# Kernel optimization log

Measured on AMD Instinct MI355X. Metric: run time of the kernel, lower is better.

Reference implementation:

```python
import jax, jax.numpy as jnp
import numpy as np

D = 200; H = 4; DH = D // H
N_ETYPE = 38; N_NTYPE = 4
B = 256; L = 1024; E = B * L
NODES_PER_G = 200; N = B * NODES_PER_G


def _bn(x, g, b):
    # BatchNorm1d in training mode: batch stats over rows (biased variance, eps=1e-5)
    m = x.mean(axis=0)
    v = x.var(axis=0)
    return (x - m) * jax.lax.rsqrt(v + 1e-5) * g + b


def setup_inputs():
    key = jax.random.key(0)
    ks = jax.random.split(key, 24)
    f = lambda k, s: jax.random.normal(k, s, jnp.float32) * 0.02
    head = jax.random.randint(ks[0], (E,), 0, N)
    tail = (head + 1 + jax.random.randint(ks[1], (E,), 0, N - 1)) % N  # guaranteed no self-loops
    return {
        "x": jax.random.normal(ks[2], (N, D), jnp.float32),
        "node_feature_extra": jax.random.normal(ks[3], (N, D), jnp.float32),
        "sent_vec_r": jax.random.normal(ks[4], (B, D), jnp.float32),
        "We1": f(ks[5], (N_ETYPE + 1 + 2 * N_NTYPE, D)), "be1": jnp.zeros((D,), jnp.float32),
        "ge1": jnp.ones((D,), jnp.float32), "bte1": jnp.zeros((D,), jnp.float32),
        "We2": f(ks[6], (D, D)), "be2": jnp.zeros((D,), jnp.float32),
        "Wa1": f(ks[7], (2 * D, D)), "ba1": jnp.zeros((D,), jnp.float32),
        "ga1": jnp.ones((D,), jnp.float32), "bta1": jnp.zeros((D,), jnp.float32),
        "Wa2": f(ks[8], (D, D)), "ba2": jnp.zeros((D,), jnp.float32),
        "Watt": f(ks[9], (D, D)),
        "Wk": f(ks[10], (2 * D, D)), "bk": jnp.zeros((D,), jnp.float32),
        "Wm": f(ks[11], (2 * D, D)), "bm": jnp.zeros((D,), jnp.float32),
        "Wq": f(ks[12], (D, D)), "bq": jnp.zeros((D,), jnp.float32),
        "Wo1": f(ks[13], (D, D)), "bo1": jnp.zeros((D,), jnp.float32),
        "go1": jnp.ones((D,), jnp.float32), "bto1": jnp.zeros((D,), jnp.float32),
        "Wo2": f(ks[14], (D, D)), "bo2": jnp.zeros((D,), jnp.float32),
        "edge_index": jnp.stack([head, tail]),
        "edge_type": jax.random.randint(ks[15], (E,), 0, N_ETYPE),
        "node_type": jax.random.randint(ks[16], (N,), 0, N_NTYPE),
        "edges_per_graph": L,
    }


def reference(x, node_feature_extra, sent_vec_r, We1, be1, ge1, bte1, We2, be2,
              Wa1, ba1, ga1, bta1, Wa2, ba2, Watt, Wk, bk, Wm, bm, Wq, bq,
              Wo1, bo1, go1, bto1, Wo2, bo2,
              edge_index, edge_type, node_type, edges_per_graph):
    E_, N_ = edge_index.shape[1], x.shape[0]
    src, dst = edge_index[0], edge_index[1]
    x_head, x_tail = x[src], x[dst]
    x_fact = x_tail - x_head
    nt = N_ETYPE + 1
    # original does this segment-mean on detached CPU numpy -> no gradient path
    xf = jax.lax.stop_gradient(x_fact)
    sums = jax.ops.segment_sum(xf, edge_type, num_segments=nt)
    cnts = jax.ops.segment_sum(jnp.ones((E_,), x.dtype), edge_type, num_segments=nt)
    result = (sums / jnp.maximum(cnts, 1.0)[:, None])[edge_type]  # [E, D]
    # one-hot edge/node-type features for real edges + self edges
    edge_vec = jax.nn.one_hot(edge_type, nt, dtype=x.dtype)
    self_edge_vec = jnp.zeros((N_, nt), x.dtype).at[:, N_ETYPE].set(1.0)
    ht = jnp.concatenate([jax.nn.one_hot(node_type[src], N_NTYPE, dtype=x.dtype),
                          jax.nn.one_hot(node_type[dst], N_NTYPE, dtype=x.dtype)], 1)
    sh = jax.nn.one_hot(node_type, N_NTYPE, dtype=x.dtype)
    feat = jnp.concatenate([jnp.concatenate([edge_vec, ht], 1),
                            jnp.concatenate([self_edge_vec, sh, sh], 1)], 0)  # [E+N, 47]
    emb = jax.nn.relu(_bn(feat @ We1 + be1, ge1, bte1)) @ We2 + be2  # edge_encoder, [E+N, D]
    emb_e, emb_self = emb[:E_], emb[E_:]
    # edge_encoder_again on cat([emb_e, result]); split matmul avoids the [E,2D] concat
    h2 = _bn(emb_e @ Wa1[:D] + result @ Wa1[D:] + ba1, ga1, bta1)
    R = jax.nn.relu(h2) @ Wa2 + ba2  # [E, D]
    # per-graph attention: Q rows within a graph are identical (repeated sent_vec),
    # so the LxL softmax has identical rows -> compute one row per graph and broadcast.
    Bg = E_ // edges_per_graph
    Rg = R.reshape(Bg, edges_per_graph, D)
    q = sent_vec_r @ Watt  # [B, D]
    scores = jnp.einsum('bd,bld->bl', q, Rg) / jnp.sqrt(jnp.asarray(D, x.dtype))
    attn = jax.nn.softmax(scores, axis=1)
    upd = jnp.einsum('bl,bld->bd', attn, Rg)
    updated_R = jnp.broadcast_to(upd[:, None, :], Rg.shape).reshape(E_, D)
    edge_attr = jnp.concatenate([updated_R, emb_self], 0)
    # append self-loops (input edge_index has none, matching remove_self_loops)
    loop = jnp.arange(N_, dtype=src.dtype)
    src_all = jnp.concatenate([src, loop])
    dst_all = jnp.concatenate([dst, loop])
    x_i, x_j = x[dst_all], x[src_all]
    key_ = (x_i @ Wk[:D] + edge_attr @ Wk[D:] + bk).reshape(-1, H, DH)
    msg = (x_j @ Wm[:D] + edge_attr @ Wm[D:] + bm).reshape(-1, H, DH)
    qry = ((x_j @ Wq + bq) / jnp.sqrt(jnp.asarray(DH, x.dtype))).reshape(-1, H, DH)
    sc = (qry * key_).sum(-1)  # [E+N, H]
    # segment softmax grouped by source node (every segment non-empty due to self-loops)
    smax = jax.ops.segment_max(sc, src_all, num_segments=N_)
    ex = jnp.exp(sc - smax[src_all])
    den = jax.ops.segment_sum(ex, src_all, num_segments=N_)
    alpha = ex / den[src_all]
    cnt = jax.ops.segment_sum(jnp.ones((src_all.shape[0],), x.dtype), src_all, num_segments=N_)
    alpha = alpha * cnt[src_all][:, None]
    m = (msg * alpha[:, :, None]).reshape(-1, D)
    aggr = jax.ops.segment_sum(m, dst_all, num_segments=N_)  # scatter-add at targets
    return jax.nn.relu(_bn(aggr @ Wo1 + bo1, go1, bto1)) @ Wo2 + bo2
```

## Files before the change

### kernel.cpp

```cpp
#include <hip/hip_runtime.h>

#define D     200
#define H     4
#define DH    50
#define NE    38
#define NTY   4
#define NC    608
#define NCT   612
#define BG    256
#define LG    1024
#define EE    262144
#define NN    51200
#define EA    313344
#define NB    200

#define NTILES 13
#define KSTEPS 7
#define NMATS  8
#define SLICE_SHORTS 13312
#define NCHUNK 26

typedef __attribute__((ext_vector_type(4))) float  f32x4;
typedef __attribute__((ext_vector_type(8))) short  bf16x8;

__device__ __forceinline__ short bf_hi(float f) {
    unsigned u = __float_as_uint(f);
    unsigned r = u + 0x7fffu + ((u >> 16) & 1u);
    return (short)(r >> 16);
}
__device__ __forceinline__ float bf_f(short s) {
    return __uint_as_float(((unsigned)(unsigned short)s) << 16);
}

__global__ __launch_bounds__(256) void k_hist(const int* __restrict__ ei, const int* __restrict__ et,
                                              const int* __restrict__ nt, int* hist, int* outdeg, int* indeg,
                                              int* hcnt) {
    int e = blockIdx.x * 256 + threadIdx.x;
    if (e >= EE) return;
    int s = ei[e], d = ei[EE + e];
    int c = et[e] * 16 + nt[s] * 4 + nt[d];
    atomicAdd(&hist[c], 1);
    atomicAdd(&outdeg[s], 1);
    atomicAdd(&indeg[d], 1);
    atomicAdd(&hcnt[(e >> 10) * NC + c], 1);
}

__global__ __launch_bounds__(256) void k_ntcnt(const int* __restrict__ nt, int* ntcnt) {
    __shared__ int loc[NTY];
    int t = threadIdx.x;
    if (t < NTY) loc[t] = 0;
    __syncthreads();
    int n = blockIdx.x * 256 + t;
    if (n < NN) atomicAdd(&loc[nt[n]], 1);
    __syncthreads();
    if (t < NTY) atomicAdd(&ntcnt[t], loc[t]);
}

__global__ void k_tcnt(const int* __restrict__ hist, int* tcnt) {
    int t = threadIdx.x;
    if (t < NE) { int s = 0; for (int i = 0; i < 16; i++) s += hist[t*16 + i]; tcnt[t] = s; }
}

__global__ __launch_bounds__(256) void k_coef(const int* __restrict__ ei, const int* __restrict__ et,
                                              float* coef) {
    int e = blockIdx.x * 256 + threadIdx.x;
    if (e >= EE) return;
    int s = ei[e], d = ei[EE + e], t = et[e];
    unsafeAtomicAdd(&coef[(size_t)d * NE + t],  1.f);
    unsafeAtomicAdd(&coef[(size_t)s * NE + t], -1.f);
}

__global__ __launch_bounds__(256) void k_xfsum3(const float* __restrict__ x, const float* __restrict__ coef,
                                                float* sums) {
    const int CH = NN / 256;
    int t = threadIdx.x;
    int n0 = blockIdx.x * CH;
    float acc[NE];
    #pragma unroll
    for (int m = 0; m < NE; m++) acc[m] = 0.f;
    if (t < D) {
        for (int k = 0; k < CH; k++) {
            int n = n0 + k;
            float xv = x[(size_t)n * D + t];
            const float* cf = coef + (size_t)n * NE;
            #pragma unroll
            for (int m = 0; m < NE; m++) acc[m] += cf[m] * xv;
        }
        #pragma unroll
        for (int m = 0; m < NE; m++)
            if (acc[m] != 0.f) unsafeAtomicAdd(&sums[m * D + t], acc[m]);
    }
}

__global__ __launch_bounds__(256) void k_scan_a(const int* __restrict__ a, const int* __restrict__ b,
                                                int* bsA, int* bsB) {
    __shared__ int redA[4], redB[4];
    int t = threadIdx.x, blk = blockIdx.x;
    int i = blk * 256 + t;
    int va = a[i], vb = b[i];
    for (int o = 1; o < 64; o <<= 1) { va += __shfl_xor(va, o); vb += __shfl_xor(vb, o); }
    int wave = t >> 6, lane = t & 63;
    if (lane == 0) { redA[wave] = va; redB[wave] = vb; }
    __syncthreads();
    if (t == 0) {
        bsA[blk] = redA[0] + redA[1] + redA[2] + redA[3];
        bsB[blk] = redB[0] + redB[1] + redB[2] + redB[3];
    }
}

__global__ __launch_bounds__(256) void k_scan_b(int* bsA, int* bsB, int* aoff, int* boff) {
    __shared__ int pa[256], pb[256];
    int t = threadIdx.x;
    int va = (t < NB) ? bsA[t] : 0;
    int vb = (t < NB) ? bsB[t] : 0;
    pa[t] = va; pb[t] = vb;
    __syncthreads();
    for (int off = 1; off < 256; off <<= 1) {
        int xa = (t >= off) ? pa[t - off] : 0;
        int xb = (t >= off) ? pb[t - off] : 0;
        __syncthreads();
        pa[t] += xa; pb[t] += xb;
        __syncthreads();
    }
    if (t < NB) { bsA[t] = pa[t] - va; bsB[t] = pb[t] - vb; }
    if (t == NB - 1) { aoff[NN] = pa[t]; boff[NN] = pb[t]; }
}

__global__ __launch_bounds__(256) void k_scan_c(const int* __restrict__ a, const int* __restrict__ b,
                                                const int* __restrict__ bsA, const int* __restrict__ bsB,
                                                int* aoff, int* boff, int* acur, int* bcur) {
    __shared__ int wsA[4], wsB[4];
    int t = threadIdx.x, blk = blockIdx.x;
    int i = blk * 256 + t;
    int va = a[i], vb = b[i];
    int wave = t >> 6, lane = t & 63;
    int sa = va, sb = vb;
    for (int o = 1; o < 64; o <<= 1) {
        int xa = __shfl_up(sa, o);
        int xb = __shfl_up(sb, o);
        if (lane >= o) { sa += xa; sb += xb; }
    }
    if (lane == 63) { wsA[wave] = sa; wsB[wave] = sb; }
    __syncthreads();
    int baseA = bsA[blk], baseB = bsB[blk];
    #pragma unroll
    for (int wv = 0; wv < 3; wv++) {
        if (wv < wave) { baseA += wsA[wv]; baseB += wsB[wv]; }
    }
    int ea = baseA + sa - va;
    int eb = baseB + sb - vb;
    aoff[i] = ea; acur[i] = ea;
    boff[i] = eb; bcur[i] = eb;
}

__global__ __launch_bounds__(256) void k_scatter(const int* __restrict__ ei, int* scur, int* dcur,
                                                 int* slist, int* dlist) {
    int e = blockIdx.x * 256 + threadIdx.x;
    if (e >= EE) return;
    int s = ei[e], d = ei[EE + e];
    slist[atomicAdd(&scur[s], 1)] = e;
    dlist[atomicAdd(&dcur[d], 1)] = e;
}

__global__ __launch_bounds__(256) void k_combos1(const float* __restrict__ We1, const float* __restrict__ be1,
                                                 const int* __restrict__ hist, const int* __restrict__ ntcnt,
                                                 float* __restrict__ h1, float* bn1) {
    int c = blockIdx.x, d = threadIdx.x;
    if (d >= D) return;
    float v, w;
    if (c < NC) {
        int etp = c >> 4, ts = (c >> 2) & 3, td = c & 3;
        v = We1[etp*D + d] + We1[(39+ts)*D + d] + We1[(43+td)*D + d] + be1[d];
        w = (float)hist[c];
    } else {
        int t = c - NC;
        v = We1[38*D + d] + We1[(39+t)*D + d] + We1[(43+t)*D + d] + be1[d];
        w = (float)ntcnt[t];
    }
    h1[c*D + d] = v;
    unsafeAtomicAdd(&bn1[d], w * v);
    unsafeAtomicAdd(&bn1[D + d], w * v * v);
}

__global__ __launch_bounds__(256) void k_combos2(const float* __restrict__ h1, const float* __restrict__ bn1,
                                                 const float* __restrict__ ge1, const float* __restrict__ bte1,
                                                 const float* __restrict__ We2, const float* __restrict__ be2,
                                                 float* __restrict__ embE, float* __restrict__ embS) {
    __shared__ float v[D];
    int c = blockIdx.x, t = threadIdx.x;
    if (t < D) {
        float cnt = (float)(EE + NN);
        float m = bn1[t] / cnt;
        float var = bn1[D + t] / cnt - m * m;
        float r = rsqrtf(var + 1e-5f);
        float u = (h1[c*D + t] - m) * r * ge1[t] + bte1[t];
        v[t] = fmaxf(u, 0.f);
    }
    __syncthreads();
    if (t < D) {
        float acc = be2[t];
        for (int k = 0; k < D; k++) acc += v[k] * We2[k*D + t];
        if (c < NC) embE[c*D + t] = acc; else embS[(c-NC)*D + t] = acc;
    }
}

__global__ __launch_bounds__(256) void k_combos3(const float* __restrict__ embE, const float* __restrict__ sumsxf,
                                                 const int* __restrict__ tcnt, const float* __restrict__ Wa1,
                                                 const float* __restrict__ ba1, const int* __restrict__ hist,
                                                 float* __restrict__ h2, float* bn2) {
    __shared__ float a[2*D];
    int c = blockIdx.x, t = threadIdx.x;
    int etp = c >> 4;
    if (t < D) {
        a[t] = embE[c*D + t];
        float cn = fmaxf((float)tcnt[etp], 1.f);
        a[D + t] = sumsxf[etp*D + t] / cn;
    }
    __syncthreads();
    if (t < D) {
        float acc = ba1[t];
        for (int k = 0; k < 2*D; k++) acc += a[k] * Wa1[k*D + t];
        h2[c*D + t] = acc;
        float w = (float)hist[c];
        unsafeAtomicAdd(&bn2[t], w * acc);
        unsafeAtomicAdd(&bn2[D + t], w * acc * acc);
    }
}

__global__ __launch_bounds__(256) void k_combos4(const float* __restrict__ h2, const float* __restrict__ bn2,
                                                 const float* __restrict__ ga1, const float* __restrict__ bta1,
                                                 const float* __restrict__ Wa2, const float* __restrict__ ba2,
                                                 float* __restrict__ Rc, float* __restrict__ RcT) {
    __shared__ float v[D];
    int c = blockIdx.x, t = threadIdx.x;
    if (t < D) {
        float inv = 1.f / (float)EE;
        float m = bn2[t] * inv;
        float var = bn2[D + t] * inv - m * m;
        float r = rsqrtf(var + 1e-5f);
        float u = (h2[c*D + t] - m) * r * ga1[t] + bta1[t];
        v[t] = fmaxf(u, 0.f);
    }
    __syncthreads();
    if (t < D) {
        float acc = ba2[t];
        for (int k = 0; k < D; k++) acc += v[k] * Wa2[k*D + t];
        Rc[c*D + t] = acc;
        RcT[(size_t)t * NC + c] = acc;
    }
}

__global__ __launch_bounds__(512) void k_attn(const float* __restrict__ qs,
                                              const float* __restrict__ Rc, const float* __restrict__ RcT,
                                              const int* __restrict__ hcnt, float* __restrict__ upd) {
    __shared__ float q[D];
    __shared__ float w[NC];
    __shared__ float red[16];
    __shared__ float part[8][D];
    int b = blockIdx.x, t = threadIdx.x;
    int wave = t >> 6, lane = t & 63;
    if (t < D) q[t] = qs[b*D + t];
    __syncthreads();
    {
        float s0a = 0.f, s0b = 0.f, s0c = 0.f, s0d = 0.f;
        float s1a = 0.f, s1b = 0.f, s1c = 0.f, s1d = 0.f;
        for (int k = 0; k < D; k += 4) {
            float q0 = q[k], q1 = q[k+1], q2 = q[k+2], q3 = q[k+3];
            const float* r = RcT + (size_t)k * NC;
            s0a += q0 * r[t];
            s0b += q1 * r[NC + t];
            s0c += q2 * r[2*NC + t];
            s0d += q3 * r[3*NC + t];
            if (t < NC - 512) {
                s1a += q0 * r[t + 512];
                s1b += q1 * r[NC + t + 512];
                s1c += q2 * r[2*NC + t + 512];
                s1d += q3 * r[3*NC + t + 512];
            }
        }
        w[t] = (s0a + s0b) + (s0c + s0d);
        if (t < NC - 512) w[t + 512] = (s1a + s1b) + (s1c + s1d);
    }
    __syncthreads();
    float mx = -1e30f;
    for (int c = t; c < NC; c += 512) mx = fmaxf(mx, w[c]);
    for (int o = 32; o; o >>= 1) mx = fmaxf(mx, __shfl_xor(mx, o));
    if (lane == 0) red[wave] = mx;
    __syncthreads();
    mx = red[0];
    #pragma unroll
    for (int i = 1; i < 8; i++) mx = fmaxf(mx, red[i]);
    float sm = 0.f;
    for (int c = t; c < NC; c += 512) {
        float wv = (float)hcnt[b * NC + c] * __expf(w[c] - mx);
        w[c] = wv;
        sm += wv;
    }
    for (int o = 32; o; o >>= 1) sm += __shfl_xor(sm, o);
    if (lane == 0) red[8 + wave] = sm;
    __syncthreads();
    float tot = red[8];
    #pragma unroll
    for (int i = 1; i < 8; i++) tot += red[8 + i];
    float inv = 1.f / tot;
    float a4[4] = {0.f, 0.f, 0.f, 0.f};
    for (int c = wave * (NC/8); c < (wave + 1) * (NC/8); c++) {
        float wv = w[c];
        const float* r = Rc + c * D;
        #pragma unroll
        for (int j = 0; j < 4; j++) { int dd = lane + 64*j; if (dd < D) a4[j] += wv * r[dd]; }
    }
    #pragma unroll
    for (int j = 0; j < 4; j++) { int dd = lane + 64*j; if (dd < D) part[wave][dd] = a4[j]; }
    __syncthreads();
    if (t < D) {
        float s = part[0][t];
        #pragma unroll
        for (int i = 1; i < 8; i++) s += part[i][t];
        upd[b*D + t] = s * inv;
    }
}

__global__ __launch_bounds__(256) void k_packW(const float* __restrict__ Wk, const float* __restrict__ Wm,
                                               const float* __restrict__ Wq, const float* __restrict__ Wo1,
                                               const float* __restrict__ Wo2, const float* __restrict__ Watt,
                                               short* __restrict__ Bpk) {
    int blk = blockIdx.x;
    int mat = blk / (NTILES * KSTEPS);
    int rem = blk - mat * (NTILES * KSTEPS);
    int ks = rem / NTILES, nt = rem - ks * NTILES;
    const float* W = (mat == 0) ? Wk : (mat == 1) ? Wm : (mat == 2) ? Wq : (mat == 3) ? Wo1 :
                     (mat == 4) ? Wo2 : (mat == 5) ? Watt : (mat == 6) ? (Wk + D*D) : (Wm + D*D);
    int t = threadIdx.x;
    for (int idx = t; idx < 1024; idx += 256) {
        int split = idx >> 9;
        int lane = (idx & 511) >> 3;
        int j = idx & 7;
        int n = nt * 16 + (lane & 15);
        int k = ks * 32 + ((lane >> 4) << 3) + j;
        float v = (k < D && n < D) ? W[k * D + n] : 0.f;
        short h = bf_hi(v);
        short out = split ? bf_hi(v - bf_f(h)) : h;
        Bpk[(size_t)blk * 1024 + idx] = out;
    }
}

__device__ __forceinline__ void stage_load(const short* __restrict__ g, int w, int lane, f32x4 rg[7]) {
    #pragma unroll
    for (int i = 0; i < 7; i++) {
        int c = w + 4 * i;
        if (c < NCHUNK) rg[i] = *(const f32x4*)((const char*)g + c * 1024 + lane * 16);
    }
}
__device__ __forceinline__ void stage_write(short* l, int w, int lane, const f32x4 rg[7]) {
    #pragma unroll
    for (int i = 0; i < 7; i++) {
        int c = w + 4 * i;
        if (c < NCHUNK) *(f32x4*)((char*)l + c * 1024 + lane * 16) = rg[i];
    }
}

__device__ __forceinline__ void load_afrag(const float* __restrict__ A, int row, int quad, int ks,
                                           int preop, const float* __restrict__ bnacc, float invCnt,
                                           const float* __restrict__ g, const float* __restrict__ bb,
                                           bf16x8& ah, bf16x8& al) {
    int k0 = ks * 32 + quad * 8;
    float v[8];
    if (k0 < D) {
        const float* src = A + (size_t)row * D + k0;
        float4 p0 = *(const float4*)src;
        float4 p1 = *(const float4*)(src + 4);
        v[0]=p0.x; v[1]=p0.y; v[2]=p0.z; v[3]=p0.w;
        v[4]=p1.x; v[5]=p1.y; v[6]=p1.z; v[7]=p1.w;
        if (preop) {
            float4 m0 = *(const float4*)(bnacc + k0);
            float4 m1 = *(const float4*)(bnacc + k0 + 4);
            float4 q0 = *(const float4*)(bnacc + D + k0);
            float4 q1 = *(const float4*)(bnacc + D + k0 + 4);
            float4 g0 = *(const float4*)(g + k0);
            float4 g1 = *(const float4*)(g + k0 + 4);
            float4 b0 = *(const float4*)(bb + k0);
            float4 b1 = *(const float4*)(bb + k0 + 4);
            float mm[8] = {m0.x,m0.y,m0.z,m0.w,m1.x,m1.y,m1.z,m1.w};
            float qq[8] = {q0.x,q0.y,q0.z,q0.w,q1.x,q1.y,q1.z,q1.w};
            float gg[8] = {g0.x,g0.y,g0.z,g0.w,g1.x,g1.y,g1.z,g1.w};
            float bv[8] = {b0.x,b0.y,b0.z,b0.w,b1.x,b1.y,b1.z,b1.w};
            #pragma unroll
            for (int j = 0; j < 8; j++) {
                float mj = mm[j] * invCnt;
                float var = qq[j] * invCnt - mj * mj;
                float rs = rsqrtf(var + 1e-5f);
                float s = rs * gg[j];
                v[j] = fmaxf(v[j] * s + (bv[j] - mj * s), 0.f);
            }
        }
    } else {
        #pragma unroll
        for (int j = 0; j < 8; j++) v[j] = 0.f;
    }
    #pragma unroll
    for (int j = 0; j < 8; j++) {
        short h = bf_hi(v[j]);
        ah[j] = h;
        al[j] = bf_hi(v[j] - bf_f(h));
    }
}

__device__ __forceinline__ void store_C(f32x4 acc[NTILES], float* __restrict__ C, int n0, int w, int lane,
                                        const float* __restrict__ bias, float postscale) {
    int colb = lane & 15, quad = lane >> 4;
    #pragma unroll
    for (int nt = 0; nt < NTILES; nt++) {
        int col = nt * 16 + colb;
        if (col < D) {
            float bj = bias ? bias[col] : 0.f;
            #pragma unroll
            for (int r = 0; r < 4; r++) {
                int row = n0 + w * 16 + quad * 4 + r;
                C[(size_t)row * D + col] = (acc[nt][r] + bj) * postscale;
            }
        }
    }
}

__global__ __launch_bounds__(256, 3) void k_mmf3(const float* __restrict__ A, const short* __restrict__ Bpk,
                                                 const float* __restrict__ bq,
                                                 float* __restrict__ XK, float* __restrict__ XM, float* __restrict__ XQ) {
    __shared__ __align__(16) short Bls[2 * SLICE_SHORTS];
    int t = threadIdx.x, w = t >> 6, lane = t & 63;
    int n0 = blockIdx.x * 64;
    int row = n0 + w * 16 + (lane & 15);
    int quad = lane >> 4;
    f32x4 rg[7];
    stage_load(Bpk, w, lane, rg);
    stage_write(Bls, w, lane, rg);
    __syncthreads();
    f32x4 acc[NTILES];
    const int NU = 3 * KSTEPS;
    for (int u = 0; u < NU; ++u) {
        int cur = u & 1;
        if (u + 1 < NU)
            stage_load(Bpk + (size_t)(u + 1) * SLICE_SHORTS, w, lane, rg);
        int mat = u / KSTEPS;
        int ks = u - mat * KSTEPS;
        bf16x8 ah, al;
        load_afrag(A, row, quad, ks, 0, nullptr, 0.f, nullptr, nullptr, ah, al);
        if (ks == 0) {
            #pragma unroll
            for (int nt = 0; nt < NTILES; nt++) { acc[nt][0]=0.f; acc[nt][1]=0.f; acc[nt][2]=0.f; acc[nt][3]=0.f; }
        }
        const bf16x8* B8 = (const bf16x8*)(Bls + cur * SLICE_SHORTS);
        #pragma unroll
        for (int nt = 0; nt < NTILES; nt++) {
            bf16x8 bh = B8[nt * 128 + lane];
            bf16x8 bl = B8[nt * 128 + 64 + lane];
            acc[nt] = __builtin_amdgcn_mfma_f32_16x16x32_bf16(al, bh, acc[nt], 0, 0, 0);
            acc[nt] = __builtin_amdgcn_mfma_f32_16x16x32_bf16(ah, bl, acc[nt], 0, 0, 0);
            acc[nt] = __builtin_amdgcn_mfma_f32_16x16x32_bf16(ah, bh, acc[nt], 0, 0, 0);
        }
        if (ks == KSTEPS - 1) {
            if (mat == 0)      store_C(acc, XK, n0, w, lane, nullptr, 1.f);
            else if (mat == 1) store_C(acc, XM, n0, w, lane, nullptr, 1.f);
            else               store_C(acc, XQ, n0, w, lane, bq, 0.14142135623730950488f);
        }
        if (u + 1 < NU) {
            stage_write(Bls + (cur ^ 1) * SLICE_SHORTS, w, lane, rg);
            __syncthreads();
        }
    }
}

__global__ __launch_bounds__(256, 3) void k_mmf(const float* __restrict__ A, const short* __restrict__ Bmat,
                                                const float* __restrict__ bias, float* __restrict__ C,
                                                int preop, const float* __restrict__ bnacc, float invCnt,
                                                const float* __restrict__ g, const float* __restrict__ bb,
                                                float postscale) {
    __shared__ __align__(16) short Bls[2 * SLICE_SHORTS];
    int t = threadIdx.x, w = t >> 6, lane = t & 63;
    int n0 = blockIdx.x * 64;
    int row = n0 + w * 16 + (lane & 15);
    int quad = lane >> 4;
    f32x4 rg[7];
    stage_load(Bmat, w, lane, rg);
    stage_write(Bls, w, lane, rg);
    __syncthreads();
    f32x4 acc[NTILES];
    #pragma unroll
    for (int nt = 0; nt < NTILES; nt++) { acc[nt][0]=0.f; acc[nt][1]=0.f; acc[nt][2]=0.f; acc[nt][3]=0.f; }
    for (int u = 0; u < KSTEPS; ++u) {
        int cur = u & 1;
        if (u + 1 < KSTEPS)
            stage_load(Bmat + (size_t)(u + 1) * SLICE_SHORTS, w, lane, rg);
        bf16x8 ah, al;
        load_afrag(A, row, quad, u, preop, bnacc, invCnt, g, bb, ah, al);
        const bf16x8* B8 = (const bf16x8*)(Bls + cur * SLICE_SHORTS);
        #pragma unroll
        for (int nt = 0; nt < NTILES; nt++) {
            bf16x8 bh = B8[nt * 128 + lane];
            bf16x8 bl = B8[nt * 128 + 64 + lane];
            acc[nt] = __builtin_amdgcn_mfma_f32_16x16x32_bf16(al, bh, acc[nt], 0, 0, 0);
            acc[nt] = __builtin_amdgcn_mfma_f32_16x16x32_bf16(ah, bl, acc[nt], 0, 0, 0);
            acc[nt] = __builtin_amdgcn_mfma_f32_16x16x32_bf16(ah, bh, acc[nt], 0, 0, 0);
        }
        if (u + 1 < KSTEPS) {
            stage_write(Bls + (cur ^ 1) * SLICE_SHORTS, w, lane, rg);
            __syncthreads();
        }
    }
    store_C(acc, C, n0, w, lane, bias, postscale);
}

__global__ __launch_bounds__(256) void k_soft(const int* __restrict__ ei, const int* __restrict__ nt,
                                              const int* __restrict__ soff, const int* __restrict__ slist,
                                              const int* __restrict__ outdeg,
                                              const float* __restrict__ XQ, const float* __restrict__ XK,
                                              const float* __restrict__ GK, const float* __restrict__ SK,
                                              float* __restrict__ sc, float* __restrict__ scale) {
    int wave = threadIdx.x >> 6, lane = threadIdx.x & 63;
    int n = blockIdx.x * 4 + wave;
    if (n >= NN) return;
    float qv[4];
    #pragma unroll
    for (int j = 0; j < 4; j++) { int dd = lane + 64*j; qv[j] = (dd < D) ? XQ[(size_t)n*D + dd] : 0.f; }
    float den0 = 0.f, den1 = 0.f, den2 = 0.f, den3 = 0.f;
    {
        int tn = nt[n];
        float h0 = 0, h1 = 0, h2 = 0, h3 = 0;
        #pragma unroll
        for (int j = 0; j < 4; j++) {
            int dd = lane + 64*j;
            if (dd < D) {
                float p = qv[j] * (XK[(size_t)n*D + dd] + SK[tn*D + dd]);
                int hh = dd / DH;
                if (hh == 0) h0 += p; else if (hh == 1) h1 += p; else if (hh == 2) h2 += p; else h3 += p;
            }
        }
        for (int o = 32; o; o >>= 1) {
            h0 += __shfl_xor(h0, o); h1 += __shfl_xor(h1, o);
            h2 += __shfl_xor(h2, o); h3 += __shfl_xor(h3, o);
        }
        float e0 = __expf(h0), e1 = __expf(h1), e2 = __expf(h2), e3 = __expf(h3);
        den0 += e0; den1 += e1; den2 += e2; den3 += e3;
        if (lane < 4) {
            float v = (lane == 0) ? e0 : (lane == 1) ? e1 : (lane == 2) ? e2 : e3;
            sc[(size_t)(EE + n) * 4 + lane] = v;
        }
    }
    int beg = soff[n], end = soff[n + 1];
    for (int i = beg; i < end; i++) {
        int e = slist[i];
        int tail = ei[EE + e];
        int g = e >> 10;
        float h0 = 0, h1 = 0, h2 = 0, h3 = 0;
        #pragma unroll
        for (int j = 0; j < 4; j++) {
            int dd = lane + 64*j;
            if (dd < D) {
                float p = qv[j] * (XK[(size_t)tail*D + dd] + GK[g*D + dd]);
                int hh = dd / DH;
                if (hh == 0) h0 += p; else if (hh == 1) h1 += p; else if (hh == 2) h2 += p; else h3 += p;
            }
        }
        for (int o = 32; o; o >>= 1) {
            h0 += __shfl_xor(h0, o); h1 += __shfl_xor(h1, o);
            h2 += __shfl_xor(h2, o); h3 += __shfl_xor(h3, o);
        }
        float e0 = __expf(h0), e1 = __expf(h1), e2 = __expf(h2), e3 = __expf(h3);
        den0 += e0; den1 += e1; den2 += e2; den3 += e3;
        if (lane < 4) {
            float v = (lane == 0) ? e0 : (lane == 1) ? e1 : (lane == 2) ? e2 : e3;
            sc[(size_t)e * 4 + lane] = v;
        }
    }
    float cnt = (float)(outdeg[n] + 1);
    if (lane < 4) {
        float dn = (lane == 0) ? den0 : (lane == 1) ? den1 : (lane == 2) ? den2 : den3;
        scale[(size_t)n * 4 + lane] = cnt / dn;
    }
}

__global__ __launch_bounds__(256) void k_aggr(const int* __restrict__ ei, const int* __restrict__ nt,
                                              const int* __restrict__ doff, const int* __restrict__ dlist,
                                              const float* __restrict__ sc, const float* __restrict__ scale,
                                              const float* __restrict__ XM, const float* __restrict__ GM,
                                              const float* __restrict__ SM, float* __restrict__ aggr) {
    int wave = threadIdx.x >> 6, lane = threadIdx.x & 63;
    int n = blockIdx.x * 4 + wave;
    if (n >= NN) return;
    float acc[4] = {0.f, 0.f, 0.f, 0.f};
    {
        int tn = nt[n];
        float4 ss = *(const float4*)&sc[(size_t)(EE + n) * 4];
        float4 sl = *(const float4*)&scale[(size_t)n * 4];
        float a0 = ss.x * sl.x, a1 = ss.y * sl.y, a2 = ss.z * sl.z, a3 = ss.w * sl.w;
        #pragma unroll
        for (int j = 0; j < 4; j++) {
            int dd = lane + 64*j;
            if (dd < D) {
                float al = (dd < DH) ? a0 : (dd < 2*DH) ? a1 : (dd < 3*DH) ? a2 : a3;
                acc[j] += al * (XM[(size_t)n*D + dd] + SM[tn*D + dd]);
            }
        }
    }
    int beg = doff[n], end = doff[n + 1];
    for (int i = beg; i < end; i++) {
        int e = dlist[i];
        int s = ei[e];
        int g = e >> 10;
        float4 ss = *(const float4*)&sc[(size_t)e * 4];
        float4 sl = *(const float4*)&scale[(size_t)s * 4];
        float a0 = ss.x * sl.x, a1 = ss.y * sl.y, a2 = ss.z * sl.z, a3 = ss.w * sl.w;
        #pragma unroll
        for (int j = 0; j < 4; j++) {
            int dd = lane + 64*j;
            if (dd < D) {
                float al = (dd < DH) ? a0 : (dd < 2*DH) ? a1 : (dd < 3*DH) ? a2 : a3;
                acc[j] += al * (XM[(size_t)s*D + dd] + GM[g*D + dd]);
            }
        }
    }
    #pragma unroll
    for (int j = 0; j < 4; j++) {
        int dd = lane + 64*j;
        if (dd < D) aggr[(size_t)n*D + dd] = acc[j];
    }
}

__global__ __launch_bounds__(256) void k_colstats(const float* __restrict__ T1, float* bn3) {
    int t = threadIdx.x;
    if (t >= D) return;
    int r0 = blockIdx.x * 256;
    float s = 0.f, q = 0.f;
    for (int r = r0; r < r0 + 256; r++) {
        float v = T1[(size_t)r * D + t];
        s += v; q += v * v;
    }
    unsafeAtomicAdd(&bn3[t], s);
    unsafeAtomicAdd(&bn3[D + t], q);
}

extern "C" void kernel_launch(void* const* d_in, const int* in_sizes, int n_in,
                              void* d_out, int out_size, void* d_ws, size_t ws_size,
                              hipStream_t stream) {
    const float* x    = (const float*)d_in[0];
    const float* sent = (const float*)d_in[2];
    const float* We1  = (const float*)d_in[3];
    const float* be1  = (const float*)d_in[4];
    const float* ge1  = (const float*)d_in[5];
    const float* bte1 = (const float*)d_in[6];
    const float* We2  = (const float*)d_in[7];
    const float* be2  = (const float*)d_in[8];
    const float* Wa1  = (const float*)d_in[9];
    const float* ba1  = (const float*)d_in[10];
    const float* ga1  = (const float*)d_in[11];
    const float* bta1 = (const float*)d_in[12];
    const float* Wa2  = (const float*)d_in[13];
    const float* ba2  = (const float*)d_in[14];
    const float* Watt = (const float*)d_in[15];
    const float* Wk   = (const float*)d_in[16];
    const float* bk   = (const float*)d_in[17];
    const float* Wm   = (const float*)d_in[18];
    const float* bm   = (const float*)d_in[19];
    const float* Wq   = (const float*)d_in[20];
    const float* bq   = (const float*)d_in[21];
    const float* Wo1  = (const float*)d_in[22];
    const float* bo1  = (const float*)d_in[23];
    const float* go1  = (const float*)d_in[24];
    const float* bto1 = (const float*)d_in[25];
    const float* Wo2  = (const float*)d_in[26];
    const float* bo2  = (const float*)d_in[27];
    const int* ei = (const int*)d_in[28];
    const int* et = (const int*)d_in[29];
    const int* nt = (const int*)d_in[30];

    char* ws = (char*)d_ws;
    size_t off = 0;
    auto alloc = [&](size_t bytes) -> char* {
        char* p = ws + off;
        off = (off + bytes + 255) & ~(size_t)255;
        return p;
    };
    int*   hist   = (int*)  alloc(NC * 4);
    int*   ntcnt  = (int*)  alloc(NTY * 4);
    float* bn1    = (float*)alloc(2 * D * 4);
    float* bn2    = (float*)alloc(2 * D * 4);
    float* bn3    = (float*)alloc(2 * D * 4);
    float* sumsxf = (float*)alloc(NE * D * 4);
    int*   outdeg = (int*)  alloc(NN * 4);
    int*   indeg  = (int*)  alloc(NN * 4);
    int*   hcnt   = (int*)  alloc((size_t)BG * NC * 4);
    float* updS   = (float*)alloc((size_t)320 * D * 4);
    size_t zero_end = off;
    int* tcnt = (int*)alloc(NE * 4);
    int* soff_ = (int*)alloc((NN + 1) * 4);
    int* doff_ = (int*)alloc((NN + 1) * 4);
    int* scur = (int*)alloc(NN * 4);
    int* dcur = (int*)alloc(NN * 4);
    int* bsA  = (int*)alloc(NB * 4);
    int* bsB  = (int*)alloc(NB * 4);
    int* slist = (int*)alloc((size_t)EE * 4);
    int* dlist = (int*)alloc((size_t)EE * 4);
    short* Bpk  = (short*)alloc((size_t)NMATS * NTILES * KSTEPS * 1024 * 2);
    float* h1v   = (float*)alloc((size_t)NCT * D * 4);
    float* embE  = (float*)alloc((size_t)NC * D * 4);
    float* h2pre = (float*)alloc((size_t)NC * D * 4);
    float* Rc    = (float*)alloc((size_t)NC * D * 4);
    float* RcT   = (float*)alloc((size_t)D * NC * 4);
    float* qs    = (float*)alloc((size_t)BG * D * 4);
    float* GK    = (float*)alloc((size_t)320 * D * 4);
    float* GM    = (float*)alloc((size_t)320 * D * 4);
    float* sc    = (float*)alloc((size_t)EA * H * 4);
    float* XK    = (float*)alloc((size_t)NN * D * 4);
    float* XM    = (float*)alloc((size_t)NN * D * 4);
    float* XQ    = (float*)alloc((size_t)NN * D * 4);
    float* coef  = XK;
    float* scale = h1v;
    float* aggr  = XQ;
    float* T1    = XK;
    float* embS  = updS + 256 * D;
    float* SK    = GK + 256 * D;
    float* SM    = GM + 256 * D;

    const int matstride = NTILES * KSTEPS * 1024;

    hipMemsetAsync(ws, 0, zero_end, stream);
    hipMemsetAsync(coef, 0, (size_t)NN * NE * 4, stream);

    k_packW  <<<NMATS * NTILES * KSTEPS, 256, 0, stream>>>(Wk, Wm, Wq, Wo1, Wo2, Watt, Bpk);
    k_hist   <<<EE / 256, 256, 0, stream>>>(ei, et, nt, hist, outdeg, indeg, hcnt);
    k_ntcnt  <<<NN / 256, 256, 0, stream>>>(nt, ntcnt);
    k_coef   <<<EE / 256, 256, 0, stream>>>(ei, et, coef);
    k_tcnt   <<<1, 64, 0, stream>>>(hist, tcnt);
    k_scan_a <<<NB, 256, 0, stream>>>(outdeg, indeg, bsA, bsB);
    k_scan_b <<<1, 256, 0, stream>>>(bsA, bsB, soff_, doff_);
    k_scan_c <<<NB, 256, 0, stream>>>(outdeg, indeg, bsA, bsB, soff_, doff_, scur, dcur);
    k_scatter<<<EE / 256, 256, 0, stream>>>(ei, scur, dcur, slist, dlist);
    k_xfsum3 <<<256, 256, 0, stream>>>(x, coef, sumsxf);
    k_mmf    <<<BG / 64, 256, 0, stream>>>(sent, Bpk + (size_t)5 * matstride, nullptr, qs,
                                           0, nullptr, 0.f, nullptr, nullptr, 0.07071067811865475f);
    k_combos1<<<NCT, 256, 0, stream>>>(We1, be1, hist, ntcnt, h1v, bn1);
    k_combos2<<<NCT, 256, 0, stream>>>(h1v, bn1, ge1, bte1, We2, be2, embE, embS);
    k_combos3<<<NC, 256, 0, stream>>>(embE, sumsxf, tcnt, Wa1, ba1, hist, h2pre, bn2);
    k_combos4<<<NC, 256, 0, stream>>>(h2pre, bn2, ga1, bta1, Wa2, ba2, Rc, RcT);
    k_attn   <<<BG, 512, 0, stream>>>(qs, Rc, RcT, hcnt, updS);
    k_mmf    <<<5, 256, 0, stream>>>(updS, Bpk + (size_t)6 * matstride, bk, GK,
                                     0, nullptr, 0.f, nullptr, nullptr, 1.f);
    k_mmf    <<<5, 256, 0, stream>>>(updS, Bpk + (size_t)7 * matstride, bm, GM,
                                     0, nullptr, 0.f, nullptr, nullptr, 1.f);
    k_mmf3   <<<NN / 64, 256, 0, stream>>>(x, Bpk, bq, XK, XM, XQ);
    k_soft   <<<NN / 4, 256, 0, stream>>>(ei, nt, soff_, slist, outdeg, XQ, XK, GK, SK, sc, scale);
    k_aggr   <<<NN / 4, 256, 0, stream>>>(ei, nt, doff_, dlist, sc, scale, XM, GM, SM, aggr);
    k_mmf    <<<NN / 64, 256, 0, stream>>>(aggr, Bpk + (size_t)3 * matstride, bo1, T1,
                                           0, nullptr, 0.f, nullptr, nullptr, 1.f);
    k_colstats<<<NN / 256, 256, 0, stream>>>(T1, bn3);
    k_mmf    <<<NN / 64, 256, 0, stream>>>(T1, Bpk + (size_t)4 * matstride, bo2, (float*)d_out,
                                           1, bn3, 1.f / (float)NN, go1, bto1, 1.f);
}
```

Measured before the change: 980.8 us.

## Use 128-row GEMM tiles with preloaded A fragments; head-aligned lanes in softmax/aggregate

The GEMM kernels now run 512 threads over 128 rows per block. Each block loads all seven A k-step fragments into registers up front, so the shared-memory B slice is reused across twice as many rows and the global A loads sit outside the k loop. The per-edge softmax and aggregation kernels now map lanes 0-49 to one dimension within each head, reading four strided values. A custom shuffle tree reduces all four heads together, replacing four separate full-wave reductions. This raises register pressure (14 bf16x8 fragments plus accumulators) and leaves 14 of 64 lanes idle in the edge kernels, and the padded buffers grow to 384 rows.

```diff
diff --git a/kernel.cpp b/kernel.cpp
--- a/kernel.cpp
+++ b/kernel.cpp
@@ -19,6 +19,7 @@
 #define NMATS  8
 #define SLICE_SHORTS 13312
 #define NCHUNK 26
+#define MROWS  128
 
 typedef __attribute__((ext_vector_type(4))) float  f32x4;
 typedef __attribute__((ext_vector_type(8))) short  bf16x8;
@@ -345,17 +346,17 @@
     }
 }
 
-__device__ __forceinline__ void stage_load(const short* __restrict__ g, int w, int lane, f32x4 rg[7]) {
-    #pragma unroll
-    for (int i = 0; i < 7; i++) {
-        int c = w + 4 * i;
+__device__ __forceinline__ void stage_load8(const short* __restrict__ g, int w, int lane, f32x4 rg[4]) {
+    #pragma unroll
+    for (int i = 0; i < 4; i++) {
+        int c = w + 8 * i;
         if (c < NCHUNK) rg[i] = *(const f32x4*)((const char*)g + c * 1024 + lane * 16);
     }
 }
-__device__ __forceinline__ void stage_write(short* l, int w, int lane, const f32x4 rg[7]) {
-    #pragma unroll
-    for (int i = 0; i < 7; i++) {
-        int c = w + 4 * i;
+__device__ __forceinline__ void stage_write8(short* l, int w, int lane, const f32x4 rg[4]) {
+    #pragma unroll
+    for (int i = 0; i < 4; i++) {
+        int c = w + 8 * i;
         if (c < NCHUNK) *(f32x4*)((char*)l + c * 1024 + lane * 16) = rg[i];
     }
 }
@@ -423,91 +424,111 @@
     }
 }
 
-__global__ __launch_bounds__(256, 3) void k_mmf3(const float* __restrict__ A, const short* __restrict__ Bpk,
+#define MMF_KS(MATV, KS, AH, AL, NUTOT, BASE)                                   \
+    {                                                                           \
+        int u_ = (MATV) * KSTEPS + (KS);                                        \
+        int cur_ = u_ & 1;                                                      \
+        if (u_ + 1 < (NUTOT))                                                   \
+            stage_load8((BASE) + (size_t)(u_ + 1) * SLICE_SHORTS, w, lane, rg); \
+        const bf16x8* B8_ = (const bf16x8*)(Bls + cur_ * SLICE_SHORTS);         \
+        _Pragma("unroll")                                                       \
+        for (int nt = 0; nt < NTILES; nt++) {                                   \
+            bf16x8 bh = B8_[nt * 128 + lane];                                   \
+            bf16x8 bl = B8_[nt * 128 + 64 + lane];                              \
+            acc[nt] = __builtin_amdgcn_mfma_f32_16x16x32_bf16(AL, bh, acc[nt], 0, 0, 0); \
+            acc[nt] = __builtin_amdgcn_mfma_f32_16x16x32_bf16(AH, bl, acc[nt], 0, 0, 0); \
+            acc[nt] = __builtin_amdgcn_mfma_f32_16x16x32_bf16(AH, bh, acc[nt], 0, 0, 0); \
+        }                                                                       \
+        if (u_ + 1 < (NUTOT)) {                                                 \
+            stage_write8(Bls + (cur_ ^ 1) * SLICE_SHORTS, w, lane, rg);         \
+            __syncthreads();                                                    \
+        }                                                                       \
+    }
+
+__global__ __launch_bounds__(512, 2) void k_mmf3(const float* __restrict__ A, const short* __restrict__ Bpk,
                                                  const float* __restrict__ bq,
                                                  float* __restrict__ XK, float* __restrict__ XM, float* __restrict__ XQ) {
     __shared__ __align__(16) short Bls[2 * SLICE_SHORTS];
     int t = threadIdx.x, w = t >> 6, lane = t & 63;
-    int n0 = blockIdx.x * 64;
+    int n0 = blockIdx.x * MROWS;
     int row = n0 + w * 16 + (lane & 15);
     int quad = lane >> 4;
-    f32x4 rg[7];
-    stage_load(Bpk, w, lane, rg);
-    stage_write(Bls, w, lane, rg);
+    bf16x8 ah0, al0, ah1, al1, ah2, al2, ah3, al3, ah4, al4, ah5, al5, ah6, al6;
+    load_afrag(A, row, quad, 0, 0, nullptr, 0.f, nullptr, nullptr, ah0, al0);
+    load_afrag(A, row, quad, 1, 0, nullptr, 0.f, nullptr, nullptr, ah1, al1);
+    load_afrag(A, row, quad, 2, 0, nullptr, 0.f, nullptr, nullptr, ah2, al2);
+    load_afrag(A, row, quad, 3, 0, nullptr, 0.f, nullptr, nullptr, ah3, al3);
+    load_afrag(A, row, quad, 4, 0, nullptr, 0.f, nullptr, nullptr, ah4, al4);
+    load_afrag(A, row, quad, 5, 0, nullptr, 0.f, nullptr, nullptr, ah5, al5);
+    load_afrag(A, row, quad, 6, 0, nullptr, 0.f, nullptr, nullptr, ah6, al6);
+    f32x4 rg[4];
+    stage_load8(Bpk, w, lane, rg);
+    stage_write8(Bls, w, lane, rg);
     __syncthreads();
     f32x4 acc[NTILES];
-    const int NU = 3 * KSTEPS;
-    for (int u = 0; u < NU; ++u) {
-        int cur = u & 1;
-        if (u + 1 < NU)
-            stage_load(Bpk + (size_t)(u + 1) * SLICE_SHORTS, w, lane, rg);
-        int mat = u / KSTEPS;
-        int ks = u - mat * KSTEPS;
-        bf16x8 ah, al;
-        load_afrag(A, row, quad, ks, 0, nullptr, 0.f, nullptr, nullptr, ah, al);
-        if (ks == 0) {
-            #pragma unroll
-            for (int nt = 0; nt < NTILES; nt++) { acc[nt][0]=0.f; acc[nt][1]=0.f; acc[nt][2]=0.f; acc[nt][3]=0.f; }
-        }
-        const bf16x8* B8 = (const bf16x8*)(Bls + cur * SLICE_SHORTS);
+    for (int mat = 0; mat < 3; ++mat) {
         #pragma unroll
-        for (int nt = 0; nt < NTILES; nt++) {
-            bf16x8 bh = B8[nt * 128 + lane];
-            bf16x8 bl = B8[nt * 128 + 64 + lane];
-            acc[nt] = __builtin_amdgcn_mfma_f32_16x16x32_bf16(al, bh, acc[nt], 0, 0, 0);
-            acc[nt] = __builtin_amdgcn_mfma_f32_16x16x32_bf16(ah, bl, acc[nt], 0, 0, 0);
-            acc[nt] = __builtin_amdgcn_mfma_f32_16x16x32_bf16(ah, bh, acc[nt], 0, 0, 0);
-        }
-        if (ks == KSTEPS - 1) {
-            if (mat == 0)      store_C(acc, XK, n0, w, lane, nullptr, 1.f);
-            else if (mat == 1) store_C(acc, XM, n0, w, lane, nullptr, 1.f);
-            else               store_C(acc, XQ, n0, w, lane, bq, 0.14142135623730950488f);
-        }
-        if (u + 1 < NU) {
-            stage_write(Bls + (cur ^ 1) * SLICE_SHORTS, w, lane, rg);
-            __syncthreads();
-        }
-    }
-}
-
-__global__ __launch_bounds__(256, 3) void k_mmf(const float* __restrict__ A, const short* __restrict__ Bmat,
+        for (int nt = 0; nt < NTILES; nt++) { acc[nt][0]=0.f; acc[nt][1]=0.f; acc[nt][2]=0.f; acc[nt][3]=0.f; }
+        MMF_KS(mat, 0, ah0, al0, 3*KSTEPS, Bpk)
+        MMF_KS(mat, 1, ah1, al1, 3*KSTEPS, Bpk)
+        MMF_KS(mat, 2, ah2, al2, 3*KSTEPS, Bpk)
+        MMF_KS(mat, 3, ah3, al3, 3*KSTEPS, Bpk)
+        MMF_KS(mat, 4, ah4, al4, 3*KSTEPS, Bpk)
+        MMF_KS(mat, 5, ah5, al5, 3*KSTEPS, Bpk)
+        MMF_KS(mat, 6, ah6, al6, 3*KSTEPS, Bpk)
+        if (mat == 0)      store_C(acc, XK, n0, w, lane, nullptr, 1.f);
+        else if (mat == 1) store_C(acc, XM, n0, w, lane, nullptr, 1.f);
+        else               store_C(acc, XQ, n0, w, lane, bq, 0.14142135623730950488f);
+    }
+}
+
+__global__ __launch_bounds__(512, 2) void k_mmf(const float* __restrict__ A, const short* __restrict__ Bmat,
                                                 const float* __restrict__ bias, float* __restrict__ C,
                                                 int preop, const float* __restrict__ bnacc, float invCnt,
                                                 const float* __restrict__ g, const float* __restrict__ bb,
                                                 float postscale) {
     __shared__ __align__(16) short Bls[2 * SLICE_SHORTS];
     int t = threadIdx.x, w = t >> 6, lane = t & 63;
-    int n0 = blockIdx.x * 64;
+    int n0 = blockIdx.x * MROWS;
     int row = n0 + w * 16 + (lane & 15);
     int quad = lane >> 4;
-    f32x4 rg[7];
-    stage_load(Bmat, w, lane, rg);
-    stage_write(Bls, w, lane, rg);
+    bf16x8 ah0, al0, ah1, al1, ah2, al2, ah3, al3, ah4, al4, ah5, al5, ah6, al6;
+    load_afrag(A, row, quad, 0, preop, bnacc, invCnt, g, bb, ah0, al0);
+    load_afrag(A, row, quad, 1, preop, bnacc, invCnt, g, bb, ah1, al1);
+    load_afrag(A, row, quad, 2, preop, bnacc, invCnt, g, bb, ah2, al2);
+    load_afrag(A, row, quad, 3, preop, bnacc, invCnt, g, bb, ah3, al3);
+    load_afrag(A, row, quad, 4, preop, bnacc, invCnt, g, bb, ah4, al4);
+    load_afrag(A, row, quad, 5, preop, bnacc, invCnt, g, bb, ah5, al5);
+    load_afrag(A, row, quad, 6, preop, bnacc, invCnt, g, bb, ah6, al6);
+    f32x4 rg[4];
+    stage_load8(Bmat, w, lane, rg);
+    stage_write8(Bls, w, lane, rg);
     __syncthreads();
     f32x4 acc[NTILES];
     #pragma unroll
     for (int nt = 0; nt < NTILES; nt++) { acc[nt][0]=0.f; acc[nt][1]=0.f; acc[nt][2]=0.f; acc[nt][3]=0.f; }
-    for (int u = 0; u < KSTEPS; ++u) {
-        int cur = u & 1;
-        if (u + 1 < KSTEPS)
-            stage_load(Bmat + (size_t)(u + 1) * SLICE_SHORTS, w, lane, rg);
-        bf16x8 ah, al;
-        load_afrag(A, row, quad, u, preop, bnacc, invCnt, g, bb, ah, al);
-        const bf16x8* B8 = (const bf16x8*)(Bls + cur * SLICE_SHORTS);
-        #pragma unroll
-        for (int nt = 0; nt < NTILES; nt++) {
-            bf16x8 bh = B8[nt * 128 + lane];
-            bf16x8 bl = B8[nt * 128 + 64 + lane];
-            acc[nt] = __builtin_amdgcn_mfma_f32_16x16x32_bf16(al, bh, acc[nt], 0, 0, 0);
-            acc[nt] = __builtin_amdgcn_mfma_f32_16x16x32_bf16(ah, bl, acc[nt], 0, 0, 0);
-            acc[nt] = __builtin_amdgcn_mfma_f32_16x16x32_bf16(ah, bh, acc[nt], 0, 0, 0);
-        }
-        if (u + 1 < KSTEPS) {
-            stage_write(Bls + (cur ^ 1) * SLICE_SHORTS, w, lane, rg);
-            __syncthreads();
-        }
-    }
+    MMF_KS(0, 0, ah0, al0, KSTEPS, Bmat)
+    MMF_KS(0, 1, ah1, al1, KSTEPS, Bmat)
+    MMF_KS(0, 2, ah2, al2, KSTEPS, Bmat)
+    MMF_KS(0, 3, ah3, al3, KSTEPS, Bmat)
+    MMF_KS(0, 4, ah4, al4, KSTEPS, Bmat)
+    MMF_KS(0, 5, ah5, al5, KSTEPS, Bmat)
+    MMF_KS(0, 6, ah6, al6, KSTEPS, Bmat)
     store_C(acc, C, n0, w, lane, bias, postscale);
+}
+
+__device__ __forceinline__ float head_reduce(float h0, float h1, float h2, float h3, int lane) {
+    float ax = (lane < 32) ? h2 : h0;
+    float ay = (lane < 32) ? h3 : h1;
+    float u0 = ((lane < 32) ? h0 : h2) + __shfl_xor(ax, 32);
+    float u1 = ((lane < 32) ? h1 : h3) + __shfl_xor(ay, 32);
+    float bx = ((lane & 16) == 0) ? u1 : u0;
+    float v  = (((lane & 16) == 0) ? u0 : u1) + __shfl_xor(bx, 16);
+    v += __shfl_xor(v, 8);
+    v += __shfl_xor(v, 4);
+    v += __shfl_xor(v, 2);
+    v += __shfl_xor(v, 1);
+    return v;
 }
 
 __global__ __launch_bounds__(256) void k_soft(const int* __restrict__ ei, const int* __restrict__ nt,
@@ -519,64 +540,51 @@
     int wave = threadIdx.x >> 6, lane = threadIdx.x & 63;
     int n = blockIdx.x * 4 + wave;
     if (n >= NN) return;
-    float qv[4];
-    #pragma unroll
-    for (int j = 0; j < 4; j++) { int dd = lane + 64*j; qv[j] = (dd < D) ? XQ[(size_t)n*D + dd] : 0.f; }
-    float den0 = 0.f, den1 = 0.f, den2 = 0.f, den3 = 0.f;
+    bool act = lane < DH;
+    int grp = lane >> 4;
+    float qv0 = 0.f, qv1 = 0.f, qv2 = 0.f, qv3 = 0.f;
+    if (act) {
+        const float* q = XQ + (size_t)n * D + lane;
+        qv0 = q[0]; qv1 = q[DH]; qv2 = q[2*DH]; qv3 = q[3*DH];
+    }
+    float den = 0.f;
     {
         int tn = nt[n];
-        float h0 = 0, h1 = 0, h2 = 0, h3 = 0;
-        #pragma unroll
-        for (int j = 0; j < 4; j++) {
-            int dd = lane + 64*j;
-            if (dd < D) {
-                float p = qv[j] * (XK[(size_t)n*D + dd] + SK[tn*D + dd]);
-                int hh = dd / DH;
-                if (hh == 0) h0 += p; else if (hh == 1) h1 += p; else if (hh == 2) h2 += p; else h3 += p;
-            }
+        float h0 = 0.f, h1 = 0.f, h2 = 0.f, h3 = 0.f;
+        if (act) {
+            const float* xk = XK + (size_t)n * D + lane;
+            const float* sk = SK + (size_t)tn * D + lane;
+            h0 = qv0 * (xk[0]    + sk[0]);
+            h1 = qv1 * (xk[DH]   + sk[DH]);
+            h2 = qv2 * (xk[2*DH] + sk[2*DH]);
+            h3 = qv3 * (xk[3*DH] + sk[3*DH]);
         }
-        for (int o = 32; o; o >>= 1) {
-            h0 += __shfl_xor(h0, o); h1 += __shfl_xor(h1, o);
-            h2 += __shfl_xor(h2, o); h3 += __shfl_xor(h3, o);
-        }
-        float e0 = __expf(h0), e1 = __expf(h1), e2 = __expf(h2), e3 = __expf(h3);
-        den0 += e0; den1 += e1; den2 += e2; den3 += e3;
-        if (lane < 4) {
-            float v = (lane == 0) ? e0 : (lane == 1) ? e1 : (lane == 2) ? e2 : e3;
-            sc[(size_t)(EE + n) * 4 + lane] = v;
-        }
+        float v = head_reduce(h0, h1, h2, h3, lane);
+        float e = __expf(v);
+        den += e;
+        if ((lane & 15) == 0) sc[(size_t)(EE + n) * 4 + grp] = e;
     }
     int beg = soff[n], end = soff[n + 1];
     for (int i = beg; i < end; i++) {
-        int e = slist[i];
-        int tail = ei[EE + e];
-        int g = e >> 10;
-        float h0 = 0, h1 = 0, h2 = 0, h3 = 0;
-        #pragma unroll
-        for (int j = 0; j < 4; j++) {
-            int dd = lane + 64*j;
-            if (dd < D) {
-                float p = qv[j] * (XK[(size_t)tail*D + dd] + GK[g*D + dd]);
-                int hh = dd / DH;
-                if (hh == 0) h0 += p; else if (hh == 1) h1 += p; else if (hh == 2) h2 += p; else h3 += p;
-            }
+        int e_ = slist[i];
+        int tail = ei[EE + e_];
+        int g = e_ >> 10;
+        float h0 = 0.f, h1 = 0.f, h2 = 0.f, h3 = 0.f;
+        if (act) {
+            const float* xk = XK + (size_t)tail * D + lane;
+            const float* gk = GK + (size_t)g * D + lane;
+            h0 = qv0 * (xk[0]    + gk[0]);
+            h1 = qv1 * (xk[DH]   + gk[DH]);
+            h2 = qv2 * (xk[2*DH] + gk[2*DH]);
+            h3 = qv3 * (xk[3*DH] + gk[3*DH]);
         }
-        for (int o = 32; o; o >>= 1) {
-            h0 += __shfl_xor(h0, o); h1 += __shfl_xor(h1, o);
-            h2 += __shfl_xor(h2, o); h3 += __shfl_xor(h3, o);
-        }
-        float e0 = __expf(h0), e1 = __expf(h1), e2 = __expf(h2), e3 = __expf(h3);
-        den0 += e0; den1 += e1; den2 += e2; den3 += e3;
-        if (lane < 4) {
-            float v = (lane == 0) ? e0 : (lane == 1) ? e1 : (lane == 2) ? e2 : e3;
-            sc[(size_t)e * 4 + lane] = v;
-        }
+        float v = head_reduce(h0, h1, h2, h3, lane);
+        float e = __expf(v);
+        den += e;
+        if ((lane & 15) == 0) sc[(size_t)e_ * 4 + grp] = e;
     }
     float cnt = (float)(outdeg[n] + 1);
-    if (lane < 4) {
-        float dn = (lane == 0) ? den0 : (lane == 1) ? den1 : (lane == 2) ? den2 : den3;
-        scale[(size_t)n * 4 + lane] = cnt / dn;
-    }
+    if ((lane & 15) == 0) scale[(size_t)n * 4 + grp] = cnt / den;
 }
 
 __global__ __launch_bounds__(256) void k_aggr(const int* __restrict__ ei, const int* __restrict__ nt,
@@ -587,19 +595,19 @@
     int wave = threadIdx.x >> 6, lane = threadIdx.x & 63;
     int n = blockIdx.x * 4 + wave;
     if (n >= NN) return;
-    float acc[4] = {0.f, 0.f, 0.f, 0.f};
+    bool act = lane < DH;
+    float acc0 = 0.f, acc1 = 0.f, acc2 = 0.f, acc3 = 0.f;
     {
         int tn = nt[n];
         float4 ss = *(const float4*)&sc[(size_t)(EE + n) * 4];
         float4 sl = *(const float4*)&scale[(size_t)n * 4];
-        float a0 = ss.x * sl.x, a1 = ss.y * sl.y, a2 = ss.z * sl.z, a3 = ss.w * sl.w;
-        #pragma unroll
-        for (int j = 0; j < 4; j++) {
-            int dd = lane + 64*j;
-            if (dd < D) {
-                float al = (dd < DH) ? a0 : (dd < 2*DH) ? a1 : (dd < 3*DH) ? a2 : a3;
-                acc[j] += al * (XM[(size_t)n*D + dd] + SM[tn*D + dd]);
-            }
+        if (act) {
+            const float* xm = XM + (size_t)n * D + lane;
+            const float* sm = SM + (size_t)tn * D + lane;
+            acc0 += ss.x * sl.x * (xm[0]    + sm[0]);
+            acc1 += ss.y * sl.y * (xm[DH]   + sm[DH]);
+            acc2 += ss.z * sl.z * (xm[2*DH] + sm[2*DH]);
+            acc3 += ss.w * sl.w * (xm[3*DH] + sm[3*DH]);
         }
     }
     int beg = doff[n], end = doff[n + 1];
@@ -609,20 +617,21 @@
         int g = e >> 10;
         float4 ss = *(const float4*)&sc[(size_t)e * 4];
         float4 sl = *(const float4*)&scale[(size_t)s * 4];
-        float a0 = ss.x * sl.x, a1 = ss.y * sl.y, a2 = ss.z * sl.z, a3 = ss.w * sl.w;
-        #pragma unroll
-        for (int j = 0; j < 4; j++) {
-            int dd = lane + 64*j;
-            if (dd < D) {
-                float al = (dd < DH) ? a0 : (dd < 2*DH) ? a1 : (dd < 3*DH) ? a2 : a3;
-                acc[j] += al * (XM[(size_t)s*D + dd] + GM[g*D + dd]);
-            }
+        if (act) {
+            const float* xm = XM + (size_t)s * D + lane;
+            const float* gm = GM + (size_t)g * D + lane;
+            acc0 += ss.x * sl.x * (xm[0]    + gm[0]);
+            acc1 += ss.y * sl.y * (xm[DH]   + gm[DH]);
+            acc2 += ss.z * sl.z * (xm[2*DH] + gm[2*DH]);
+            acc3 += ss.w * sl.w * (xm[3*DH] + gm[3*DH]);
         }
     }
-    #pragma unroll
-    for (int j = 0; j < 4; j++) {
-        int dd = lane + 64*j;
-        if (dd < D) aggr[(size_t)n*D + dd] = acc[j];
+    if (act) {
+        float* out = aggr + (size_t)n * D + lane;
+        out[0]    = acc0;
+        out[DH]   = acc1;
+        out[2*DH] = acc2;
+        out[3*DH] = acc3;
     }
 }
 
@@ -689,7 +698,7 @@
     int*   outdeg = (int*)  alloc(NN * 4);
     int*   indeg  = (int*)  alloc(NN * 4);
     int*   hcnt   = (int*)  alloc((size_t)BG * NC * 4);
-    float* updS   = (float*)alloc((size_t)320 * D * 4);
+    float* updS   = (float*)alloc((size_t)384 * D * 4);
     size_t zero_end = off;
     int* tcnt = (int*)alloc(NE * 4);
     int* soff_ = (int*)alloc((NN + 1) * 4);
@@ -707,8 +716,8 @@
     float* Rc    = (float*)alloc((size_t)NC * D * 4);
     float* RcT   = (float*)alloc((size_t)D * NC * 4);
     float* qs    = (float*)alloc((size_t)BG * D * 4);
-    float* GK    = (float*)alloc((size_t)320 * D * 4);
-    float* GM    = (float*)alloc((size_t)320 * D * 4);
+    float* GK    = (float*)alloc((size_t)384 * D * 4);
+    float* GM    = (float*)alloc((size_t)384 * D * 4);
     float* sc    = (float*)alloc((size_t)EA * H * 4);
     float* XK    = (float*)alloc((size_t)NN * D * 4);
     float* XM    = (float*)alloc((size_t)NN * D * 4);
@@ -736,23 +745,23 @@
     k_scan_c <<<NB, 256, 0, stream>>>(outdeg, indeg, bsA, bsB, soff_, doff_, scur, dcur);
     k_scatter<<<EE / 256, 256, 0, stream>>>(ei, scur, dcur, slist, dlist);
     k_xfsum3 <<<256, 256, 0, stream>>>(x, coef, sumsxf);
-    k_mmf    <<<BG / 64, 256, 0, stream>>>(sent, Bpk + (size_t)5 * matstride, nullptr, qs,
-                                           0, nullptr, 0.f, nullptr, nullptr, 0.07071067811865475f);
+    k_mmf    <<<BG / MROWS, 512, 0, stream>>>(sent, Bpk + (size_t)5 * matstride, nullptr, qs,
+                                              0, nullptr, 0.f, nullptr, nullptr, 0.07071067811865475f);
     k_combos1<<<NCT, 256, 0, stream>>>(We1, be1, hist, ntcnt, h1v, bn1);
     k_combos2<<<NCT, 256, 0, stream>>>(h1v, bn1, ge1, bte1, We2, be2, embE, embS);
     k_combos3<<<NC, 256, 0, stream>>>(embE, sumsxf, tcnt, Wa1, ba1, hist, h2pre, bn2);
     k_combos4<<<NC, 256, 0, stream>>>(h2pre, bn2, ga1, bta1, Wa2, ba2, Rc, RcT);
     k_attn   <<<BG, 512, 0, stream>>>(qs, Rc, RcT, hcnt, updS);
-    k_mmf    <<<5, 256, 0, stream>>>(updS, Bpk + (size_t)6 * matstride, bk, GK,
+    k_mmf    <<<3, 512, 0, stream>>>(updS, Bpk + (size_t)6 * matstride, bk, GK,
                                      0, nullptr, 0.f, nullptr, nullptr, 1.f);
-    k_mmf    <<<5, 256, 0, stream>>>(updS, Bpk + (size_t)7 * matstride, bm, GM,
+    k_mmf    <<<3, 512, 0, stream>>>(updS, Bpk + (size_t)7 * matstride, bm, GM,
                                      0, nullptr, 0.f, nullptr, nullptr, 1.f);
-    k_mmf3   <<<NN / 64, 256, 0, stream>>>(x, Bpk, bq, XK, XM, XQ);
+    k_mmf3   <<<NN / MROWS, 512, 0, stream>>>(x, Bpk, bq, XK, XM, XQ);
     k_soft   <<<NN / 4, 256, 0, stream>>>(ei, nt, soff_, slist, outdeg, XQ, XK, GK, SK, sc, scale);
     k_aggr   <<<NN / 4, 256, 0, stream>>>(ei, nt, doff_, dlist, sc, scale, XM, GM, SM, aggr);
-    k_mmf    <<<NN / 64, 256, 0, stream>>>(aggr, Bpk + (size_t)3 * matstride, bo1, T1,
-                                           0, nullptr, 0.f, nullptr, nullptr, 1.f);
+    k_mmf    <<<NN / MROWS, 512, 0, stream>>>(aggr, Bpk + (size_t)3 * matstride, bo1, T1,
+                                              0, nullptr, 0.f, nullptr, nullptr, 1.f);
     k_colstats<<<NN / 256, 256, 0, stream>>>(T1, bn3);
-    k_mmf    <<<NN / 64, 256, 0, stream>>>(T1, Bpk + (size_t)4 * matstride, bo2, (float*)d_out,
-                                           1, bn3, 1.f / (float)NN, go1, bto1, 1.f);
-}
+    k_mmf    <<<NN / MROWS, 512, 0, stream>>>(T1, Bpk + (size_t)4 * matstride, bo2, (float*)d_out,
+                                              1, bn3, 1.f / (float)NN, go1, bto1, 1.f);
+}
```

Result: faster. 918.3 us (-6.4%).
